# Performance work log

Measured on AMD Instinct MI355X. Metric: run time of the kernel, lower is better.

The kernel has to match this reference:

```python
import jax, jax.numpy as jnp
import numpy as np

B, S, D_MODEL, H = 2, 2048, 1024, 16
D = D_MODEL // H  # 64 per-head dim


def setup_inputs() -> dict:
    key = jax.random.key(0)
    ks = jax.random.split(key, 9)
    scale = 1.0 / np.sqrt(D_MODEL)
    x = jax.random.normal(ks[0], (B, S, D_MODEL), dtype=jnp.float32)
    # per-head Q/K/V linears stacked: [H, d_model, d] weights, [H, d] biases
    Wq = jax.random.uniform(ks[1], (H, D_MODEL, D), jnp.float32, -scale, scale)
    bq = jax.random.uniform(ks[2], (H, D), jnp.float32, -scale, scale)
    Wk = jax.random.uniform(ks[3], (H, D_MODEL, D), jnp.float32, -scale, scale)
    bk = jax.random.uniform(ks[4], (H, D), jnp.float32, -scale, scale)
    Wv = jax.random.uniform(ks[5], (H, D_MODEL, D), jnp.float32, -scale, scale)
    bv = jax.random.uniform(ks[6], (H, D), jnp.float32, -scale, scale)
    # output projection: [d_model, d_model] weight, [d_model] bias
    Wo = jax.random.uniform(ks[7], (D_MODEL, D_MODEL), jnp.float32, -scale, scale)
    bo = jax.random.uniform(ks[8], (D_MODEL,), jnp.float32, -scale, scale)
    return {"x": x, "Wq": Wq, "bq": bq, "Wk": Wk, "bk": bk,
            "Wv": Wv, "bv": bv, "Wo": Wo, "bo": bo}


def reference(x, Wq, bq, Wk, bk, Wv, bv, Wo, bo):
    # batched per-head projections (equivalent to H separate nn.Linear's)
    Q = jnp.einsum('bsm,hmd->bhsd', x, Wq) + bq[None, :, None, :]
    K = jnp.einsum('bsm,hmd->bhsd', x, Wk) + bk[None, :, None, :]
    V = jnp.einsum('bsm,hmd->bhsd', x, Wv) + bv[None, :, None, :]
    scores = jnp.einsum('bhsd,bhtd->bhst', Q, K) / jnp.sqrt(jnp.float32(D))
    attn = jax.nn.softmax(scores, axis=-1)  # [B,H,S,S]
    out = jnp.einsum('bhst,bhtd->bhsd', attn, V)
    # concat heads along feature dim: [B,S,H*D]
    out = out.transpose(0, 2, 1, 3).reshape(B, S, D_MODEL)
    # output projection; dropout is identity in eval mode
    return out @ Wo + bo
```

## Files before the change

kernel.cpp:

```cpp
#include <hip/hip_runtime.h>
#include <hip/hip_bf16.h>

#define DEV __device__ __forceinline__

typedef unsigned short u16;
typedef __attribute__((ext_vector_type(8))) short bf16x8;
typedef __attribute__((ext_vector_type(4))) float f32x4;
typedef __attribute__((ext_vector_type(16))) float f32x16;
typedef __attribute__((ext_vector_type(4))) unsigned short us4;
typedef __attribute__((ext_vector_type(2))) unsigned u32x2;

DEV void gld_lds16(const void* g, void* l) {
  __builtin_amdgcn_global_load_lds((const __attribute__((address_space(1))) void*)g,
                                   (__attribute__((address_space(3))) void*)l, 16, 0, 0);
}

DEV u16 f2bf(float x) {
  union { float f; unsigned u; } v; v.f = x;
  unsigned r = v.u + 0x7FFFu + ((v.u >> 16) & 1u);
  return (u16)(r >> 16);
}

DEV float ex2(float x) {
  float r; asm("v_exp_f32 %0, %1" : "=v"(r) : "v"(x)); return r;
}

DEV unsigned cvtpk(float a, float b) {
  unsigned r; asm("v_cvt_pk_bf16_f32 %0, %1, %2" : "=v"(r) : "v"(a), "v"(b)); return r;
}

__global__ __launch_bounds__(256) void k_cast_x(const float* __restrict__ x, u16* __restrict__ xb) {
  int i = (blockIdx.x * 256 + threadIdx.x) * 4;
  const float4 v = *(const float4*)(x + i);
  us4 o; o.x = f2bf(v.x); o.y = f2bf(v.y); o.z = f2bf(v.z); o.w = f2bf(v.w);
  *(us4*)(xb + i) = o;
}

__global__ __launch_bounds__(256) void k_prep_w(const float* __restrict__ Wq, const float* __restrict__ Wk,
                                                const float* __restrict__ Wv, const float* __restrict__ Wo,
                                                u16* __restrict__ wqkt, u16* __restrict__ wvt,
                                                u16* __restrict__ wot) {
  __shared__ float t[64][65];
  const int bb = blockIdx.x, tid = threadIdx.x;
  const float* src; u16* dst; int src_ld, dst_row0, dst_col0;
  if (bb < 768) {
    int which = bb >> 8, h = (bb >> 4) & 15, m0 = (bb & 15) * 64;
    const float* W = which == 0 ? Wq : (which == 1 ? Wk : Wv);
    src = W + h * 65536 + m0 * 64; src_ld = 64;
    dst = (which == 2) ? wvt : (wqkt + (which == 1 ? (1024 * 1024) : 0));
    dst_row0 = h * 64; dst_col0 = m0;
  } else {
    int t2 = bb - 768, mt = t2 >> 4, nt = t2 & 15;
    src = Wo + (size_t)(mt * 64) * 1024 + nt * 64; src_ld = 1024;
    dst = wot; dst_row0 = nt * 64; dst_col0 = mt * 64;
  }
  {
    int r = tid >> 2, c0 = (tid & 3) * 16;
    const float* s = src + (size_t)r * src_ld + c0;
#pragma unroll
    for (int q = 0; q < 4; ++q) {
      float4 v = *(const float4*)(s + q * 4);
      t[r][c0 + q * 4 + 0] = v.x; t[r][c0 + q * 4 + 1] = v.y;
      t[r][c0 + q * 4 + 2] = v.z; t[r][c0 + q * 4 + 3] = v.w;
    }
  }
  __syncthreads();
  {
    int d = tid >> 2, mb = (tid & 3) * 16;
    bf16x8 v0, v1;
#pragma unroll
    for (int e = 0; e < 8; ++e) {
      v0[e] = (short)f2bf(t[mb + e][d]);
      v1[e] = (short)f2bf(t[mb + 8 + e][d]);
    }
    u16* dp = dst + (size_t)(dst_row0 + d) * 1024 + dst_col0 + mb;
    *(bf16x8*)(dp) = v0;
    *(bf16x8*)(dp + 8) = v1;
  }
}

template <int MODE>
__global__ __launch_bounds__(256) void k_gemm(const u16* __restrict__ A, const u16* __restrict__ Bt,
                                              const float* __restrict__ b0, const float* __restrict__ b1,
                                              u16* __restrict__ outb, float* __restrict__ outf) {
  constexpr int K = 1024;
  __shared__ __align__(16) u16 As[2][128 * 64];
  __shared__ __align__(16) u16 Bs[2][128 * 64];
  const int tid = threadIdx.x, wid = tid >> 6, lane = tid & 63;
  const int lo = lane & 15, hi = lane >> 4;
  const int wr = wid >> 1, wc = wid & 1;
  const int bm = blockIdx.y, bn = blockIdx.x;
  const u16* Ab = A + (size_t)bm * 128 * K;
  const u16* Bb = Bt + (size_t)bn * 128 * K;
  const int sr = lane >> 3, sc = lane & 7;
  f32x4 acc[4][4] = {};

#pragma unroll
  for (int i = 0; i < 4; ++i) {
    int r = wid * 32 + i * 8 + sr;
    int cs = sc ^ (r & 7);
    gld_lds16(Ab + (size_t)r * K + cs * 8, &As[0][(wid * 32 + i * 8) * 64]);
    gld_lds16(Bb + (size_t)r * K + cs * 8, &Bs[0][(wid * 32 + i * 8) * 64]);
  }

  int cur = 0;
  for (int kt = 0; kt < 16; ++kt) {
    asm volatile("s_waitcnt vmcnt(0)" ::: "memory");
    __builtin_amdgcn_s_barrier();
    if (kt + 1 < 16) {
      const int k0 = (kt + 1) * 64;
#pragma unroll
      for (int i = 0; i < 4; ++i) {
        int r = wid * 32 + i * 8 + sr;
        int cs = sc ^ (r & 7);
        gld_lds16(Ab + (size_t)r * K + k0 + cs * 8, &As[cur ^ 1][(wid * 32 + i * 8) * 64]);
        gld_lds16(Bb + (size_t)r * K + k0 + cs * 8, &Bs[cur ^ 1][(wid * 32 + i * 8) * 64]);
      }
    }
#pragma unroll
    for (int ks = 0; ks < 2; ++ks) {
      bf16x8 af[4], bfr[4];
#pragma unroll
      for (int mt = 0; mt < 4; ++mt) {
        int r = wr * 64 + mt * 16 + lo;
        int c = (hi + 4 * ks) ^ (r & 7);
        af[mt] = *(const bf16x8*)(&As[cur][r * 64 + c * 8]);
      }
#pragma unroll
      for (int nt = 0; nt < 4; ++nt) {
        int r = wc * 64 + nt * 16 + lo;
        int c = (hi + 4 * ks) ^ (r & 7);
        bfr[nt] = *(const bf16x8*)(&Bs[cur][r * 64 + c * 8]);
      }
#pragma unroll
      for (int mt = 0; mt < 4; ++mt)
#pragma unroll
        for (int nt = 0; nt < 4; ++nt)
          acc[mt][nt] = __builtin_amdgcn_mfma_f32_16x16x32_bf16(af[mt], bfr[nt], acc[mt][nt], 0, 0, 0);
    }
    cur ^= 1;
  }
#pragma unroll
  for (int mt = 0; mt < 4; ++mt) {
#pragma unroll
    for (int nt = 0; nt < 4; ++nt) {
      const int i0 = bm * 128 + wr * 64 + mt * 16 + hi * 4;
      const int j = bn * 128 + wc * 64 + nt * 16 + lo;
#pragma unroll
      for (int rg = 0; rg < 4; ++rg) {
        const int i = i0 + rg;
        float v = acc[mt][nt][rg];
        if (MODE == 0) {
          v += (j < 1024) ? b0[j] : b1[j - 1024];
          if (j < 1024) v *= 0.18033688011112042f;
          outb[(size_t)i * 2048 + j] = f2bf(v);
        } else if (MODE == 1) {
          v += b0[i];
          outb[(size_t)((j >> 11) * 1024 + i) * 2048 + (j & 2047)] = f2bf(v);
        } else {
          v += b0[j];
          outf[(size_t)i * 1024 + j] = v;
        }
      }
    }
  }
}

__global__ __launch_bounds__(256, 3) void k_attn(const u16* __restrict__ qk, const u16* __restrict__ vt,
                                                 u16* __restrict__ ao) {
  __shared__ __align__(16) u16 Kl[3][64 * 64];
  __shared__ __align__(16) u16 Vl[3][64 * 64];
  const int tid = threadIdx.x, wid = tid >> 6, lane = tid & 63;
  const int ql = lane & 31, Lh = lane >> 5;
  const int qb = blockIdx.x & 15, bh = blockIdx.x >> 4;
  const int b = bh >> 4, h = bh & 15;
  const int qg = qb * 128 + wid * 32 + ql;

  bf16x8 qB[4];
  const u16* qrow = qk + (size_t)(b * 2048 + qg) * 2048 + h * 64;
#pragma unroll
  for (int kd = 0; kd < 4; ++kd) qB[kd] = *(const bf16x8*)(qrow + kd * 16 + Lh * 8);

  const u16* Kg = qk + 1024 + (size_t)b * 2048 * 2048 + h * 64;
  const u16* Vg = vt + (size_t)bh * 64 * 2048;
  const int sr = lane >> 3, sc = lane & 7;

  f32x16 acco[2] = {};
  float m_run = -1e30f, l_part = 0.f;

#pragma unroll
  for (int t = 0; t < 2; ++t)
#pragma unroll
    for (int i = 0; i < 2; ++i) {
      int r = wid * 16 + i * 8 + sr;
      int cs = sc ^ (r & 7);
      gld_lds16(Kg + (size_t)(t * 64 + r) * 2048 + cs * 8, &Kl[t][(wid * 16 + i * 8) * 64]);
      gld_lds16(Vg + (size_t)r * 2048 + t * 64 + cs * 8, &Vl[t][(wid * 16 + i * 8) * 64]);
    }

  int cur = 0;
  for (int it = 0; it < 32; ++it) {
    if (it < 31) asm volatile("s_waitcnt vmcnt(4)" ::: "memory");
    else         asm volatile("s_waitcnt vmcnt(0)" ::: "memory");
    __builtin_amdgcn_s_barrier();
    if (it + 2 < 32) {
      int sb = cur + 2; if (sb >= 3) sb -= 3;
      const int t0 = (it + 2) * 64;
#pragma unroll
      for (int i = 0; i < 2; ++i) {
        int r = wid * 16 + i * 8 + sr;
        int cs = sc ^ (r & 7);
        gld_lds16(Kg + (size_t)(t0 + r) * 2048 + cs * 8, &Kl[sb][(wid * 16 + i * 8) * 64]);
        gld_lds16(Vg + (size_t)r * 2048 + t0 + cs * 8, &Vl[sb][(wid * 16 + i * 8) * 64]);
      }
    }
    const u16* Kb = Kl[cur];
    const u16* Vb = Vl[cur];

    f32x16 accs[2] = {};
#pragma unroll
    for (int kd = 0; kd < 4; ++kd) {
      int cg = 2 * kd + Lh;
#pragma unroll
      for (int tt = 0; tt < 2; ++tt) {
        int r = tt * 32 + ql;
        bf16x8 ka = *(const bf16x8*)(Kb + r * 64 + ((cg ^ (r & 7)) * 8));
        accs[tt] = __builtin_amdgcn_mfma_f32_32x32x16_bf16(ka, qB[kd], accs[tt], 0, 0, 0);
      }
    }

    bf16x8 vf[2][4];
#pragma unroll
    for (int dt = 0; dt < 2; ++dt)
#pragma unroll
      for (int kt = 0; kt < 4; ++kt) {
        int r = dt * 32 + ql;
        int cg = 2 * kt + Lh;
        vf[dt][kt] = *(const bf16x8*)(Vb + r * 64 + ((cg ^ (r & 7)) * 8));
      }

    float t8[8];
#pragma unroll
    for (int m = 0; m < 8; ++m)
      t8[m] = fmaxf(fmaxf(accs[0][2 * m], accs[0][2 * m + 1]),
                    fmaxf(accs[1][2 * m], accs[1][2 * m + 1]));
    float mx = fmaxf(fmaxf(fmaxf(t8[0], t8[1]), fmaxf(t8[2], t8[3])),
                     fmaxf(fmaxf(t8[4], t8[5]), fmaxf(t8[6], t8[7])));

    if (__any(mx > m_run + 8.f)) {
      float mxw = fmaxf(mx, __shfl_xor(mx, 32));
      float mnew = fmaxf(m_run, mxw);
      float al = ex2(m_run - mnew);
      m_run = mnew;
      l_part *= al;
      acco[0] *= al;
      acco[1] *= al;
    }

    unsigned dw[2][8];
    float ls0 = 0.f, ls1 = 0.f;
#pragma unroll
    for (int tt = 0; tt < 2; ++tt)
#pragma unroll
      for (int m = 0; m < 8; ++m) {
        float p0 = ex2(accs[tt][2 * m] - m_run);
        float p1 = ex2(accs[tt][2 * m + 1] - m_run);
        if (m & 1) ls1 += p0 + p1; else ls0 += p0 + p1;
        dw[tt][m] = cvtpk(p0, p1);
      }
    l_part += ls0 + ls1;

#pragma unroll
    for (int kt = 0; kt < 4; ++kt) {
      const int tt = kt >> 1, c = kt & 1;
      u32x2 s0 = __builtin_amdgcn_permlane32_swap(dw[tt][4 * c + 0], dw[tt][4 * c + 2], false, false);
      u32x2 s1 = __builtin_amdgcn_permlane32_swap(dw[tt][4 * c + 1], dw[tt][4 * c + 3], false, false);
      union { unsigned u[4]; bf16x8 v; } pb;
      pb.u[0] = s0[0]; pb.u[1] = s1[0]; pb.u[2] = s0[1]; pb.u[3] = s1[1];
#pragma unroll
      for (int dt = 0; dt < 2; ++dt)
        acco[dt] = __builtin_amdgcn_mfma_f32_32x32x16_bf16(vf[dt][kt], pb.v, acco[dt], 0, 0, 0);
    }

    cur = (cur == 2) ? 0 : cur + 1;
  }

  float lsum = l_part + __shfl_xor(l_part, 32);
  float inv = 1.f / lsum;
  u16* orow = ao + (size_t)(b * 2048 + qg) * 1024 + h * 64;
#pragma unroll
  for (int dt = 0; dt < 2; ++dt)
#pragma unroll
    for (int g = 0; g < 4; ++g) {
      float o0 = acco[dt][4 * g + 0] * inv, o1 = acco[dt][4 * g + 1] * inv;
      float o2 = acco[dt][4 * g + 2] * inv, o3 = acco[dt][4 * g + 3] * inv;
      uint2 w; w.x = cvtpk(o0, o1); w.y = cvtpk(o2, o3);
      *(uint2*)(orow + dt * 32 + g * 8 + Lh * 4) = w;
    }
}

extern "C" void kernel_launch(void* const* d_in, const int* in_sizes, int n_in,
                              void* d_out, int out_size, void* d_ws, size_t ws_size,
                              hipStream_t stream) {
  const float* x  = (const float*)d_in[0];
  const float* Wq = (const float*)d_in[1];
  const float* bq = (const float*)d_in[2];
  const float* Wk = (const float*)d_in[3];
  const float* bk = (const float*)d_in[4];
  const float* Wv = (const float*)d_in[5];
  const float* bv = (const float*)d_in[6];
  const float* Wo = (const float*)d_in[7];
  const float* bo = (const float*)d_in[8];
  float* out = (float*)d_out;

  char* ws = (char*)d_ws;
  u16* xb   = (u16*)(ws);
  u16* wqkt = (u16*)(ws + (8u << 20));
  u16* wvt  = (u16*)(ws + (12u << 20));
  u16* wot  = (u16*)(ws + (14u << 20));
  u16* qk   = (u16*)(ws + (16u << 20));
  u16* vt   = (u16*)(ws + (32u << 20));
  u16* aob  = (u16*)(ws + (40u << 20));

  k_cast_x<<<4096, 256, 0, stream>>>(x, xb);
  k_prep_w<<<1024, 256, 0, stream>>>(Wq, Wk, Wv, Wo, wqkt, wvt, wot);
  k_gemm<0><<<dim3(16, 32), 256, 0, stream>>>(xb, wqkt, bq, bk, qk, nullptr);
  k_gemm<1><<<dim3(32, 8), 256, 0, stream>>>(wvt, xb, bv, nullptr, vt, nullptr);
  k_attn<<<512, 256, 0, stream>>>(qk, vt, aob);
  k_gemm<2><<<dim3(8, 32), 256, 0, stream>>>(aob, wot, bo, nullptr, nullptr, out);
}
```

Measured before the change: 135.1 us.

## Fuse QKV projection into one GEMM and register-buffer K/V in attention

Merges the separate QK and V projection GEMMs into one launch whose epilogue writes V transposed, removing a launch and a second read of x. The attention kernel drops LDS staging and barriers and instead loads K/V fragments straight from global memory into registers with two-stage double buffering. It also remaps block indices so blocks of the same head spread across XCDs, and lowers the occupancy hint from 3 to 2 blocks. The risks are more VGPR pressure, global loads that no longer coalesce through LDS, and K/V reuse between waves that now has to come from cache.

Result: slower. 203.2 us (+50.4%).

```diff
diff --git a/kernel.cpp b/kernel.cpp
--- a/kernel.cpp
+++ b/kernel.cpp
@@ -38,8 +38,7 @@
 
 __global__ __launch_bounds__(256) void k_prep_w(const float* __restrict__ Wq, const float* __restrict__ Wk,
                                                 const float* __restrict__ Wv, const float* __restrict__ Wo,
-                                                u16* __restrict__ wqkt, u16* __restrict__ wvt,
-                                                u16* __restrict__ wot) {
+                                                u16* __restrict__ wqkvt, u16* __restrict__ wot) {
   __shared__ float t[64][65];
   const int bb = blockIdx.x, tid = threadIdx.x;
   const float* src; u16* dst; int src_ld, dst_row0, dst_col0;
@@ -47,7 +46,7 @@
     int which = bb >> 8, h = (bb >> 4) & 15, m0 = (bb & 15) * 64;
     const float* W = which == 0 ? Wq : (which == 1 ? Wk : Wv);
     src = W + h * 65536 + m0 * 64; src_ld = 64;
-    dst = (which == 2) ? wvt : (wqkt + (which == 1 ? (1024 * 1024) : 0));
+    dst = wqkvt + which * (1024 * 1024);
     dst_row0 = h * 64; dst_col0 = m0;
   } else {
     int t2 = bb - 768, mt = t2 >> 4, nt = t2 & 15;
@@ -82,7 +81,9 @@
 template <int MODE>
 __global__ __launch_bounds__(256) void k_gemm(const u16* __restrict__ A, const u16* __restrict__ Bt,
                                               const float* __restrict__ b0, const float* __restrict__ b1,
-                                              u16* __restrict__ outb, float* __restrict__ outf) {
+                                              const float* __restrict__ b2,
+                                              u16* __restrict__ outb, u16* __restrict__ outv,
+                                              float* __restrict__ outf) {
   constexpr int K = 1024;
   __shared__ __align__(16) u16 As[2][128 * 64];
   __shared__ __align__(16) u16 Bs[2][128 * 64];
@@ -146,33 +147,37 @@
     for (int nt = 0; nt < 4; ++nt) {
       const int i0 = bm * 128 + wr * 64 + mt * 16 + hi * 4;
       const int j = bn * 128 + wc * 64 + nt * 16 + lo;
-#pragma unroll
-      for (int rg = 0; rg < 4; ++rg) {
-        const int i = i0 + rg;
-        float v = acc[mt][nt][rg];
-        if (MODE == 0) {
-          v += (j < 1024) ? b0[j] : b1[j - 1024];
-          if (j < 1024) v *= 0.18033688011112042f;
-          outb[(size_t)i * 2048 + j] = f2bf(v);
-        } else if (MODE == 1) {
-          v += b0[i];
-          outb[(size_t)((j >> 11) * 1024 + i) * 2048 + (j & 2047)] = f2bf(v);
+      if (MODE == 0) {
+        if (j < 2048) {
+#pragma unroll
+          for (int rg = 0; rg < 4; ++rg) {
+            float v = acc[mt][nt][rg];
+            v += (j < 1024) ? b0[j] : b1[j - 1024];
+            if (j < 1024) v *= 0.18033688011112042f;
+            outb[(size_t)(i0 + rg) * 2048 + j] = f2bf(v);
+          }
         } else {
-          v += b0[j];
-          outf[(size_t)i * 1024 + j] = v;
+          const float bb2 = b2[j - 2048];
+          uint2 w;
+          w.x = cvtpk(acc[mt][nt][0] + bb2, acc[mt][nt][1] + bb2);
+          w.y = cvtpk(acc[mt][nt][2] + bb2, acc[mt][nt][3] + bb2);
+          *(uint2*)(outv + (size_t)((i0 >> 11) * 1024 + (j - 2048)) * 2048 + (i0 & 2047)) = w;
         }
+      } else {
+#pragma unroll
+        for (int rg = 0; rg < 4; ++rg)
+          outf[(size_t)(i0 + rg) * 1024 + j] = acc[mt][nt][rg] + b0[j];
       }
     }
   }
 }
 
-__global__ __launch_bounds__(256, 3) void k_attn(const u16* __restrict__ qk, const u16* __restrict__ vt,
+__global__ __launch_bounds__(256, 2) void k_attn(const u16* __restrict__ qk, const u16* __restrict__ vt,
                                                  u16* __restrict__ ao) {
-  __shared__ __align__(16) u16 Kl[3][64 * 64];
-  __shared__ __align__(16) u16 Vl[3][64 * 64];
   const int tid = threadIdx.x, wid = tid >> 6, lane = tid & 63;
   const int ql = lane & 31, Lh = lane >> 5;
-  const int qb = blockIdx.x & 15, bh = blockIdx.x >> 4;
+  const int logical = (blockIdx.x & 7) * 64 + (blockIdx.x >> 3);
+  const int qb = logical & 15, bh = logical >> 4;
   const int b = bh >> 4, h = bh & 15;
   const int qg = qb * 128 + wid * 32 + ql;
 
@@ -183,107 +188,77 @@
 
   const u16* Kg = qk + 1024 + (size_t)b * 2048 * 2048 + h * 64;
   const u16* Vg = vt + (size_t)bh * 64 * 2048;
-  const int sr = lane >> 3, sc = lane & 7;
 
   f32x16 acco[2] = {};
   float m_run = -1e30f, l_part = 0.f;
 
-#pragma unroll
-  for (int t = 0; t < 2; ++t)
-#pragma unroll
-    for (int i = 0; i < 2; ++i) {
-      int r = wid * 16 + i * 8 + sr;
-      int cs = sc ^ (r & 7);
-      gld_lds16(Kg + (size_t)(t * 64 + r) * 2048 + cs * 8, &Kl[t][(wid * 16 + i * 8) * 64]);
-      gld_lds16(Vg + (size_t)r * 2048 + t * 64 + cs * 8, &Vl[t][(wid * 16 + i * 8) * 64]);
-    }
-
-  int cur = 0;
-  for (int it = 0; it < 32; ++it) {
-    if (it < 31) asm volatile("s_waitcnt vmcnt(4)" ::: "memory");
-    else         asm volatile("s_waitcnt vmcnt(0)" ::: "memory");
-    __builtin_amdgcn_s_barrier();
-    if (it + 2 < 32) {
-      int sb = cur + 2; if (sb >= 3) sb -= 3;
-      const int t0 = (it + 2) * 64;
-#pragma unroll
-      for (int i = 0; i < 2; ++i) {
-        int r = wid * 16 + i * 8 + sr;
-        int cs = sc ^ (r & 7);
-        gld_lds16(Kg + (size_t)(t0 + r) * 2048 + cs * 8, &Kl[sb][(wid * 16 + i * 8) * 64]);
-        gld_lds16(Vg + (size_t)r * 2048 + t0 + cs * 8, &Vl[sb][(wid * 16 + i * 8) * 64]);
-      }
-    }
-    const u16* Kb = Kl[cur];
-    const u16* Vb = Vl[cur];
-
-    f32x16 accs[2] = {};
-#pragma unroll
-    for (int kd = 0; kd < 4; ++kd) {
-      int cg = 2 * kd + Lh;
-#pragma unroll
-      for (int tt = 0; tt < 2; ++tt) {
-        int r = tt * 32 + ql;
-        bf16x8 ka = *(const bf16x8*)(Kb + r * 64 + ((cg ^ (r & 7)) * 8));
-        accs[tt] = __builtin_amdgcn_mfma_f32_32x32x16_bf16(ka, qB[kd], accs[tt], 0, 0, 0);
-      }
-    }
-
-    bf16x8 vf[2][4];
-#pragma unroll
-    for (int dt = 0; dt < 2; ++dt)
-#pragma unroll
-      for (int kt = 0; kt < 4; ++kt) {
-        int r = dt * 32 + ql;
-        int cg = 2 * kt + Lh;
-        vf[dt][kt] = *(const bf16x8*)(Vb + r * 64 + ((cg ^ (r & 7)) * 8));
-      }
-
-    float t8[8];
-#pragma unroll
-    for (int m = 0; m < 8; ++m)
-      t8[m] = fmaxf(fmaxf(accs[0][2 * m], accs[0][2 * m + 1]),
-                    fmaxf(accs[1][2 * m], accs[1][2 * m + 1]));
-    float mx = fmaxf(fmaxf(fmaxf(t8[0], t8[1]), fmaxf(t8[2], t8[3])),
-                     fmaxf(fmaxf(t8[4], t8[5]), fmaxf(t8[6], t8[7])));
-
-    if (__any(mx > m_run + 8.f)) {
-      float mxw = fmaxf(mx, __shfl_xor(mx, 32));
-      float mnew = fmaxf(m_run, mxw);
-      float al = ex2(m_run - mnew);
-      m_run = mnew;
-      l_part *= al;
-      acco[0] *= al;
-      acco[1] *= al;
-    }
-
-    unsigned dw[2][8];
-    float ls0 = 0.f, ls1 = 0.f;
-#pragma unroll
-    for (int tt = 0; tt < 2; ++tt)
-#pragma unroll
-      for (int m = 0; m < 8; ++m) {
-        float p0 = ex2(accs[tt][2 * m] - m_run);
-        float p1 = ex2(accs[tt][2 * m + 1] - m_run);
-        if (m & 1) ls1 += p0 + p1; else ls0 += p0 + p1;
-        dw[tt][m] = cvtpk(p0, p1);
-      }
-    l_part += ls0 + ls1;
-
-#pragma unroll
-    for (int kt = 0; kt < 4; ++kt) {
-      const int tt = kt >> 1, c = kt & 1;
-      u32x2 s0 = __builtin_amdgcn_permlane32_swap(dw[tt][4 * c + 0], dw[tt][4 * c + 2], false, false);
-      u32x2 s1 = __builtin_amdgcn_permlane32_swap(dw[tt][4 * c + 1], dw[tt][4 * c + 3], false, false);
-      union { unsigned u[4]; bf16x8 v; } pb;
-      pb.u[0] = s0[0]; pb.u[1] = s1[0]; pb.u[2] = s0[1]; pb.u[3] = s1[1];
-#pragma unroll
-      for (int dt = 0; dt < 2; ++dt)
-        acco[dt] = __builtin_amdgcn_mfma_f32_32x32x16_bf16(vf[dt][kt], pb.v, acco[dt], 0, 0, 0);
-    }
-
-    cur = (cur == 2) ? 0 : cur + 1;
-  }
+  bf16x8 kA[8], vA[8], kB[8], vB[8];
+
+#define LOADK(KF, T0)                                                                  \
+  _Pragma("unroll") for (int kd = 0; kd < 4; ++kd) _Pragma("unroll")                   \
+      for (int tt = 0; tt < 2; ++tt)                                                   \
+          KF[kd * 2 + tt] = *(const bf16x8*)(Kg + (size_t)((T0) + tt * 32 + ql) * 2048 \
+                                             + kd * 16 + Lh * 8);
+#define LOADV(VF, T0)                                                                  \
+  _Pragma("unroll") for (int dt = 0; dt < 2; ++dt) _Pragma("unroll")                   \
+      for (int kt = 0; kt < 4; ++kt)                                                   \
+          VF[dt * 4 + kt] = *(const bf16x8*)(Vg + (size_t)(dt * 32 + ql) * 2048        \
+                                             + (T0) + kt * 16 + Lh * 8);
+#define STEP(KF, VF)                                                                   \
+  {                                                                                    \
+    f32x16 accs0 = {}, accs1 = {};                                                     \
+    _Pragma("unroll") for (int kd = 0; kd < 4; ++kd) {                                 \
+      accs0 = __builtin_amdgcn_mfma_f32_32x32x16_bf16(KF[kd * 2 + 0], qB[kd], accs0, 0, 0, 0); \
+      accs1 = __builtin_amdgcn_mfma_f32_32x32x16_bf16(KF[kd * 2 + 1], qB[kd], accs1, 0, 0, 0); \
+    }                                                                                  \
+    float t8[8];                                                                       \
+    _Pragma("unroll") for (int m = 0; m < 8; ++m)                                      \
+        t8[m] = fmaxf(fmaxf(accs0[2 * m], accs0[2 * m + 1]),                           \
+                      fmaxf(accs1[2 * m], accs1[2 * m + 1]));                          \
+    float mx = fmaxf(fmaxf(fmaxf(t8[0], t8[1]), fmaxf(t8[2], t8[3])),                  \
+                     fmaxf(fmaxf(t8[4], t8[5]), fmaxf(t8[6], t8[7])));                 \
+    if (__any(mx > m_run + 8.f)) {                                                     \
+      float mxw = fmaxf(mx, __shfl_xor(mx, 32));                                       \
+      float mnew = fmaxf(m_run, mxw);                                                  \
+      float al = ex2(m_run - mnew);                                                    \
+      m_run = mnew; l_part *= al; acco[0] *= al; acco[1] *= al;                        \
+    }                                                                                  \
+    unsigned dw0[8], dw1[8];                                                           \
+    float ls0 = 0.f, ls1 = 0.f;                                                        \
+    _Pragma("unroll") for (int m = 0; m < 8; ++m) {                                    \
+      float p0 = ex2(accs0[2 * m] - m_run), p1 = ex2(accs0[2 * m + 1] - m_run);        \
+      float p2 = ex2(accs1[2 * m] - m_run), p3 = ex2(accs1[2 * m + 1] - m_run);        \
+      ls0 += p0 + p1; ls1 += p2 + p3;                                                  \
+      dw0[m] = cvtpk(p0, p1); dw1[m] = cvtpk(p2, p3);                                  \
+    }                                                                                  \
+    l_part += ls0 + ls1;                                                               \
+    _Pragma("unroll") for (int kt = 0; kt < 4; ++kt) {                                 \
+      const int c = kt & 1;                                                            \
+      unsigned w0, w1, w2, w3;                                                         \
+      if (kt < 2) { w0 = dw0[4 * c + 0]; w1 = dw0[4 * c + 2];                          \
+                    w2 = dw0[4 * c + 1]; w3 = dw0[4 * c + 3]; }                        \
+      else        { w0 = dw1[4 * c + 0]; w1 = dw1[4 * c + 2];                          \
+                    w2 = dw1[4 * c + 1]; w3 = dw1[4 * c + 3]; }                        \
+      u32x2 s0 = __builtin_amdgcn_permlane32_swap(w0, w1, false, false);               \
+      u32x2 s1 = __builtin_amdgcn_permlane32_swap(w2, w3, false, false);               \
+      union { unsigned u[4]; bf16x8 v; } pb;                                           \
+      pb.u[0] = s0[0]; pb.u[1] = s1[0]; pb.u[2] = s0[1]; pb.u[3] = s1[1];              \
+      acco[0] = __builtin_amdgcn_mfma_f32_32x32x16_bf16(VF[0 * 4 + kt], pb.v, acco[0], 0, 0, 0); \
+      acco[1] = __builtin_amdgcn_mfma_f32_32x32x16_bf16(VF[1 * 4 + kt], pb.v, acco[1], 0, 0, 0); \
+    }                                                                                  \
+  }
+
+  LOADK(kA, 0) LOADV(vA, 0)
+#pragma unroll 1
+  for (int it = 0; it < 32; it += 2) {
+    LOADK(kB, (it + 1) * 64) LOADV(vB, (it + 1) * 64)
+    STEP(kA, vA)
+    if (it + 2 < 32) { LOADK(kA, (it + 2) * 64) LOADV(vA, (it + 2) * 64) }
+    STEP(kB, vB)
+  }
+#undef LOADK
+#undef LOADV
+#undef STEP
 
   float lsum = l_part + __shfl_xor(l_part, 32);
   float inv = 1.f / lsum;
@@ -314,18 +289,16 @@
   float* out = (float*)d_out;
 
   char* ws = (char*)d_ws;
-  u16* xb   = (u16*)(ws);
-  u16* wqkt = (u16*)(ws + (8u << 20));
-  u16* wvt  = (u16*)(ws + (12u << 20));
-  u16* wot  = (u16*)(ws + (14u << 20));
-  u16* qk   = (u16*)(ws + (16u << 20));
-  u16* vt   = (u16*)(ws + (32u << 20));
-  u16* aob  = (u16*)(ws + (40u << 20));
+  u16* xb    = (u16*)(ws);
+  u16* wqkvt = (u16*)(ws + (8u << 20));
+  u16* wot   = (u16*)(ws + (14u << 20));
+  u16* qk    = (u16*)(ws + (16u << 20));
+  u16* vt    = (u16*)(ws + (32u << 20));
+  u16* aob   = (u16*)(ws + (40u << 20));
 
   k_cast_x<<<4096, 256, 0, stream>>>(x, xb);
-  k_prep_w<<<1024, 256, 0, stream>>>(Wq, Wk, Wv, Wo, wqkt, wvt, wot);
-  k_gemm<0><<<dim3(16, 32), 256, 0, stream>>>(xb, wqkt, bq, bk, qk, nullptr);
-  k_gemm<1><<<dim3(32, 8), 256, 0, stream>>>(wvt, xb, bv, nullptr, vt, nullptr);
+  k_prep_w<<<1024, 256, 0, stream>>>(Wq, Wk, Wv, Wo, wqkvt, wot);
+  k_gemm<0><<<dim3(24, 32), 256, 0, stream>>>(xb, wqkvt, bq, bk, bv, qk, vt, nullptr);
   k_attn<<<512, 256, 0, stream>>>(qk, vt, aob);
-  k_gemm<2><<<dim3(8, 32), 256, 0, stream>>>(aob, wot, bo, nullptr, nullptr, out);
-}
+  k_gemm<2><<<dim3(8, 32), 256, 0, stream>>>(aob, wot, bo, nullptr, nullptr, nullptr, nullptr, out);
+}
```
